# Kernel tuning notes

Hardware: AMD Instinct MI355X
Metric: run time of the kernel (lower is better)

The kernel has to match this reference:

```python
import jax, jax.numpy as jnp
import numpy as np

NUM_CLASSES = 80
LAMBDA_OBJ, LAMBDA_NOOBJ, LAMBDA_BBOX, LAMBDA_CLASS = 1.0, 0.5, 5.0, 1.0
IOU_POS = 0.5
ALPHA, GAMMA = 0.25, 2.0


def setup_inputs() -> dict:
    key = jax.random.key(0)
    ks = jax.random.split(key, 7)
    B, A, H, W, C, M = 8, 3, 80, 80, NUM_CLASSES, 100
    objectness = jax.random.uniform(ks[0], (B, A, H, W, 1), dtype=jnp.float32)
    xy = jax.random.uniform(ks[1], (B, A, H, W, 2), dtype=jnp.float32)
    wh = 0.05 + 0.25 * jax.random.uniform(ks[2], (B, A, H, W, 2), dtype=jnp.float32)
    boxes = jnp.concatenate([xy, wh], axis=-1)  # (cx,cy,w,h)
    class_scores = jax.random.normal(ks[3], (B, A, H, W, C), dtype=jnp.float32)
    txy = jax.random.uniform(ks[4], (B, M, 2), dtype=jnp.float32)
    twh = 0.05 + 0.25 * jax.random.uniform(ks[5], (B, M, 2), dtype=jnp.float32)
    target_boxes = jnp.concatenate([txy, twh], axis=-1)
    target_labels = jax.random.randint(ks[6], (B, M), 0, C)
    return {"objectness": objectness, "boxes": boxes, "class_scores": class_scores,
            "target_boxes": target_boxes, "target_labels": target_labels}


def _box_iou(b1, b2):
    # b1: [N,4], b2: [M,4] in (cx,cy,w,h) -> IoU [N,M]
    b1_lo = b1[:, :2] - b1[:, 2:] * 0.5
    b1_hi = b1[:, :2] + b1[:, 2:] * 0.5
    b2_lo = b2[:, :2] - b2[:, 2:] * 0.5
    b2_hi = b2[:, :2] + b2[:, 2:] * 0.5
    lo = jnp.maximum(b1_lo[:, None, :], b2_lo[None, :, :])
    hi = jnp.minimum(b1_hi[:, None, :], b2_hi[None, :, :])
    wh = jnp.clip(hi - lo, 0.0)
    inter = wh[..., 0] * wh[..., 1]
    a1 = b1[:, 2] * b1[:, 3]
    a2 = b2[:, 2] * b2[:, 3]
    union = a1[:, None] + a2[None, :] - inter
    return inter / (union + 1e-6)


def _giou(b1, b2):
    # elementwise pairs [N,4],[N,4] -> [N]
    b1_lo = b1[:, :2] - b1[:, 2:] * 0.5
    b1_hi = b1[:, :2] + b1[:, 2:] * 0.5
    b2_lo = b2[:, :2] - b2[:, 2:] * 0.5
    b2_hi = b2[:, :2] + b2[:, 2:] * 0.5
    wh = jnp.clip(jnp.minimum(b1_hi, b2_hi) - jnp.maximum(b1_lo, b2_lo), 0.0)
    inter = wh[:, 0] * wh[:, 1]
    union = b1[:, 2] * b1[:, 3] + b2[:, 2] * b2[:, 3] - inter
    iou = inter / (union + 1e-6)
    ewh = jnp.clip(jnp.maximum(b1_hi, b2_hi) - jnp.minimum(b1_lo, b2_lo), 0.0)
    enclose = ewh[:, 0] * ewh[:, 1]
    return iou - (enclose - union) / (enclose + 1e-6)


def _per_image(obj, boxes, cls, tb, tl):
    # obj:[N], boxes:[N,4], cls:[N,C], tb:[M,4], tl:[M]
    N = boxes.shape[0]
    iou = _box_iou(boxes, tb)                 # [N,M] -- dominant intermediate
    max_iou = jnp.max(iou, axis=1)
    idx = jnp.argmax(iou, axis=1)
    pos = max_iou >= IOU_POS
    posf = pos.astype(boxes.dtype)
    bbox_t = tb[idx] * posf[:, None]          # zeros for negatives
    class_t = jnp.where(pos, tl[idx], 0)
    # objectness BCE (torch BCELoss clamps log terms at -100), summed over anchors
    logp = jnp.maximum(jnp.log(obj), -100.0)
    log1mp = jnp.maximum(jnp.log1p(-obj), -100.0)
    bce_sum = -jnp.sum(posf * logp + (1.0 - posf) * log1mp)
    pos_cnt = jnp.sum(posf)
    # faithful to source: scalar BCE sum broadcast over masks then re-summed
    obj_term = bce_sum * (LAMBDA_OBJ * pos_cnt + LAMBDA_NOOBJ * (N - pos_cnt))
    # GIoU bbox loss over positive anchors
    giou = _giou(boxes, bbox_t)
    bbox_sum = jnp.sum((1.0 - giou) * posf)
    # focal loss (logits) vs one-hot, mean over positive subset [P,C]
    onehot = jax.nn.one_hot(class_t, NUM_CLASSES, dtype=cls.dtype)
    p = jax.nn.sigmoid(cls)
    ce = jnp.maximum(cls, 0.0) - cls * onehot + jnp.log1p(jnp.exp(-jnp.abs(cls)))
    p_t = p * onehot + (1.0 - p) * (1.0 - onehot)
    a_t = ALPHA * onehot + (1.0 - ALPHA) * (1.0 - onehot)
    fl = a_t * (1.0 - p_t) ** GAMMA * ce
    class_sum = jnp.sum(fl * posf[:, None]) / jnp.maximum(pos_cnt * NUM_CLASSES, 1.0)
    return obj_term, bbox_sum, class_sum, pos_cnt


def _forward(objectness, boxes, class_scores, target_boxes, target_labels):
    B = objectness.shape[0]
    obj_f = objectness.reshape(B, -1)
    box_f = boxes.reshape(B, -1, 4)
    cls_f = class_scores.reshape(B, -1, NUM_CLASSES)
    o, bb, cl, pc = jax.vmap(_per_image)(obj_f, box_f, cls_f, target_boxes, target_labels)
    num_pos = jnp.maximum(jnp.sum(pc), 1.0)
    obj_loss = jnp.sum(o) / B
    bbox_loss = LAMBDA_BBOX * jnp.sum(bb) / num_pos
    class_loss = LAMBDA_CLASS * jnp.sum(cl) / B
    return obj_loss + bbox_loss + class_loss


def reference(objectness, boxes, class_scores, target_boxes, target_labels):
    return _forward(objectness, boxes, class_scores, target_boxes, target_labels)
```

## Files before the change

kernel.cpp:

```cpp
#include <hip/hip_runtime.h>
#include <math.h>

#define NCLS    80
#define MTGT    100
#define NANCH   19200
#define BATCH   8
#define BLKA    64
#define NBLK    (NANCH / BLKA)
#define NWAVE   4
#define TSLICE  (MTGT / NWAVE)

__device__ __forceinline__ float fast_rcp(float x) { return __builtin_amdgcn_rcpf(x); }

__device__ __forceinline__ float focal_term(float x, bool is_t) {
    const float ax  = fabsf(x);
    const float q   = __expf(-ax);
    const float ce0 = fmaxf(x, 0.0f) + __logf(1.0f + q);
    const float r   = fast_rcp(1.0f + q);
    const float p   = (x >= 0.0f) ? r : q * r;
    const float pt  = is_t ? (1.0f - p) : p;
    const float ce  = is_t ? (ce0 - x) : ce0;
    const float at  = is_t ? 0.25f : 0.75f;
    return at * pt * pt * ce;
}

__global__ __launch_bounds__(256) void anchor_kernel(
    const float* __restrict__ obj, const float* __restrict__ boxes,
    const float* __restrict__ cls, const float* __restrict__ tb,
    const int* __restrict__ tl, float4* __restrict__ partials)
{
    __shared__ float4 t_box[MTGT];
    __shared__ float  t_area[MTGT];
    __shared__ int    t_lab[MTGT];
    __shared__ float  m_bi[NWAVE][BLKA];
    __shared__ float  m_bu[NWAVE][BLKA];
    __shared__ int    m_ix[NWAVE][BLKA];

    const int b    = blockIdx.y;
    const int tid  = threadIdx.x;
    const int wave = tid >> 6;
    const int lane = tid & 63;

    if (tid < MTGT) {
        const float4 t = ((const float4*)tb)[b * MTGT + tid];
        t_box[tid]  = make_float4(t.x - 0.5f * t.z, t.y - 0.5f * t.w,
                                  t.x + 0.5f * t.z, t.y + 0.5f * t.w);
        t_area[tid] = t.z * t.w;
        t_lab[tid]  = tl[b * MTGT + tid];
    }
    __syncthreads();

    const int a   = blockIdx.x * BLKA + lane;
    const int gid = b * NANCH + a;

    const float4 bx = ((const float4*)boxes)[gid];
    const float lox = bx.x - 0.5f * bx.z, loy = bx.y - 0.5f * bx.w;
    const float hix = bx.x + 0.5f * bx.z, hiy = bx.y + 0.5f * bx.w;
    const float a1  = bx.z * bx.w;
    const float aa  = a1 + 1e-6f;

    float bi = -1.0f, bu = 1.0f; int bidx = 0;
    const int m0 = wave * TSLICE;
    #pragma unroll
    for (int mm = 0; mm < TSLICE; ++mm) {
        const int m = m0 + mm;
        const float4 t = t_box[m];
        float iw = fmaxf(fminf(hix, t.z) - fmaxf(lox, t.x), 0.0f);
        float ih = fmaxf(fminf(hiy, t.w) - fmaxf(loy, t.y), 0.0f);
        float inter = iw * ih;
        float uni   = aa + t_area[m] - inter;
        if (inter * bu > bi * uni) { bi = inter; bu = uni; bidx = m; }
    }
    m_bi[wave][lane] = bi;
    m_bu[wave][lane] = bu;
    m_ix[wave][lane] = bidx;
    __syncthreads();

    if (wave != 0) return;

    float Bi = m_bi[0][lane], Bu = m_bu[0][lane]; int Bx = m_ix[0][lane];
    #pragma unroll
    for (int w = 1; w < NWAVE; ++w) {
        const float ci = m_bi[w][lane], cu = m_bu[w][lane];
        if (ci * Bu > Bi * cu) { Bi = ci; Bu = cu; Bx = m_ix[w][lane]; }
    }

    const bool  pos  = (Bi + Bi >= Bu);
    const float posf = pos ? 1.0f : 0.0f;

    const float o   = obj[gid];
    const float bce = -fmaxf(__logf(pos ? o : 1.0f - o), -100.0f);

    float bbox_l = 0.0f;
    float focal  = 0.0f;
    if (pos) {
        const float4 t   = t_box[Bx];
        const float uni  = a1 + t_area[Bx] - Bi;
        const float iou  = Bi * fast_rcp(Bu);
        const float ew   = fmaxf(fmaxf(hix, t.z) - fminf(lox, t.x), 0.0f);
        const float eh   = fmaxf(fmaxf(hiy, t.w) - fminf(loy, t.y), 0.0f);
        const float enc  = ew * eh;
        const float giou = iou - (enc - uni) * fast_rcp(enc + 1e-6f);
        bbox_l = 1.0f - giou;

        const int c = t_lab[Bx];
        const float4* row = (const float4*)(cls + (long)gid * NCLS);
        #pragma unroll
        for (int j4 = 0; j4 < NCLS / 4; ++j4) {
            const float4 v = row[j4];
            focal += focal_term(v.x, 4 * j4 + 0 == c);
            focal += focal_term(v.y, 4 * j4 + 1 == c);
            focal += focal_term(v.z, 4 * j4 + 2 == c);
            focal += focal_term(v.w, 4 * j4 + 3 == c);
        }
    }

    float v0 = bce, v1 = posf, v2 = bbox_l, v3 = focal;
    #pragma unroll
    for (int off = 32; off; off >>= 1) {
        v0 += __shfl_down(v0, off);
        v1 += __shfl_down(v1, off);
        v2 += __shfl_down(v2, off);
        v3 += __shfl_down(v3, off);
    }
    if (lane == 0)
        partials[b * NBLK + blockIdx.x] = make_float4(v0, v1, v2, v3);
}

__global__ __launch_bounds__(512) void finalize_kernel(
    const float4* __restrict__ partials, float* __restrict__ out)
{
    const int wave = threadIdx.x >> 6;
    const int lane = threadIdx.x & 63;

    float s0 = 0.f, s1 = 0.f, s2 = 0.f, s3 = 0.f;
    for (int blk = lane; blk < NBLK; blk += 64) {
        const float4 p = partials[wave * NBLK + blk];
        s0 += p.x; s1 += p.y; s2 += p.z; s3 += p.w;
    }
    #pragma unroll
    for (int off = 32; off; off >>= 1) {
        s0 += __shfl_down(s0, off);
        s1 += __shfl_down(s1, off);
        s2 += __shfl_down(s2, off);
        s3 += __shfl_down(s3, off);
    }
    __shared__ float img[BATCH][4];
    if (lane == 0) { img[wave][0] = s0; img[wave][1] = s1; img[wave][2] = s2; img[wave][3] = s3; }
    __syncthreads();
    if (threadIdx.x == 0) {
        float sum_pc = 0.f, obj_l = 0.f, bbox_s = 0.f, cls_l = 0.f;
        #pragma unroll
        for (int b = 0; b < BATCH; ++b) {
            const float bce = img[b][0];
            const float pc  = img[b][1];
            const float bb  = img[b][2];
            const float fo  = img[b][3];
            sum_pc += pc;
            obj_l  += bce * (1.0f * pc + 0.5f * ((float)NANCH - pc));
            bbox_s += bb;
            cls_l  += fo / fmaxf(pc * (float)NCLS, 1.0f);
        }
        const float num_pos = fmaxf(sum_pc, 1.0f);
        out[0] = obj_l / (float)BATCH + 5.0f * bbox_s / num_pos + cls_l / (float)BATCH;
    }
}

extern "C" void kernel_launch(void* const* d_in, const int* in_sizes, int n_in,
                              void* d_out, int out_size, void* d_ws, size_t ws_size,
                              hipStream_t stream) {
    const float* obj   = (const float*)d_in[0];
    const float* boxes = (const float*)d_in[1];
    const float* cls   = (const float*)d_in[2];
    const float* tb    = (const float*)d_in[3];
    const int*   tl    = (const int*)d_in[4];
    float* out = (float*)d_out;

    float4* partials = (float4*)d_ws;

    dim3 gridA(NBLK, BATCH);
    anchor_kernel<<<gridA, 256, 0, stream>>>(obj, boxes, cls, tb, tl, partials);
    finalize_kernel<<<1, 512, 0, stream>>>(partials, out);
}
```

Baseline: 115.1 us.

## Spread focal-loss class-row work across all four waves with coalesced loads

The focal class loss for positive anchors now runs on all 256 threads instead of only wave 0. Each thread handles a flat (anchor, float4-chunk) index, so the 64x80 class block is read with coalesced vector loads. Wave 0 still does the argmax merge, BCE and GIoU, and publishes per-anchor positive flags and labels through shared memory. This adds an extra barrier and a shared-memory reduction in exchange for better load coalescing and less serial per-thread work.

```diff
diff --git a/kernel.cpp b/kernel.cpp
--- a/kernel.cpp
+++ b/kernel.cpp
@@ -9,6 +9,7 @@
 #define NBLK    (NANCH / BLKA)
 #define NWAVE   4
 #define TSLICE  (MTGT / NWAVE)
+#define ROW4    (NCLS / 4)
 
 __device__ __forceinline__ float fast_rcp(float x) { return __builtin_amdgcn_rcpf(x); }
 
@@ -35,6 +36,10 @@
     __shared__ float  m_bi[NWAVE][BLKA];
     __shared__ float  m_bu[NWAVE][BLKA];
     __shared__ int    m_ix[NWAVE][BLKA];
+    __shared__ float  s_posf[BLKA];
+    __shared__ int    s_lab[BLKA];
+    __shared__ float  s_foc[NWAVE];
+    __shared__ float  s_bpb[3];
 
     const int b    = blockIdx.y;
     const int tid  = threadIdx.x;
@@ -50,8 +55,8 @@
     }
     __syncthreads();
 
-    const int a   = blockIdx.x * BLKA + lane;
-    const int gid = b * NANCH + a;
+    const int a0  = blockIdx.x * BLKA;
+    const int gid = b * NANCH + a0 + lane;
 
     const float4 bx = ((const float4*)boxes)[gid];
     const float lox = bx.x - 0.5f * bx.z, loy = bx.y - 0.5f * bx.w;
@@ -76,55 +81,74 @@
     m_ix[wave][lane] = bidx;
     __syncthreads();
 
-    if (wave != 0) return;
-
-    float Bi = m_bi[0][lane], Bu = m_bu[0][lane]; int Bx = m_ix[0][lane];
-    #pragma unroll
-    for (int w = 1; w < NWAVE; ++w) {
-        const float ci = m_bi[w][lane], cu = m_bu[w][lane];
-        if (ci * Bu > Bi * cu) { Bi = ci; Bu = cu; Bx = m_ix[w][lane]; }
-    }
-
-    const bool  pos  = (Bi + Bi >= Bu);
-    const float posf = pos ? 1.0f : 0.0f;
-
-    const float o   = obj[gid];
-    const float bce = -fmaxf(__logf(pos ? o : 1.0f - o), -100.0f);
-
-    float bbox_l = 0.0f;
-    float focal  = 0.0f;
-    if (pos) {
-        const float4 t   = t_box[Bx];
-        const float uni  = a1 + t_area[Bx] - Bi;
-        const float iou  = Bi * fast_rcp(Bu);
-        const float ew   = fmaxf(fmaxf(hix, t.z) - fminf(lox, t.x), 0.0f);
-        const float eh   = fmaxf(fmaxf(hiy, t.w) - fminf(loy, t.y), 0.0f);
-        const float enc  = ew * eh;
-        const float giou = iou - (enc - uni) * fast_rcp(enc + 1e-6f);
-        bbox_l = 1.0f - giou;
-
-        const int c = t_lab[Bx];
-        const float4* row = (const float4*)(cls + (long)gid * NCLS);
+    if (wave == 0) {
+        float Bi = m_bi[0][lane], Bu = m_bu[0][lane]; int Bx = m_ix[0][lane];
         #pragma unroll
-        for (int j4 = 0; j4 < NCLS / 4; ++j4) {
-            const float4 v = row[j4];
-            focal += focal_term(v.x, 4 * j4 + 0 == c);
-            focal += focal_term(v.y, 4 * j4 + 1 == c);
-            focal += focal_term(v.z, 4 * j4 + 2 == c);
-            focal += focal_term(v.w, 4 * j4 + 3 == c);
-        }
-    }
-
-    float v0 = bce, v1 = posf, v2 = bbox_l, v3 = focal;
-    #pragma unroll
-    for (int off = 32; off; off >>= 1) {
-        v0 += __shfl_down(v0, off);
-        v1 += __shfl_down(v1, off);
-        v2 += __shfl_down(v2, off);
-        v3 += __shfl_down(v3, off);
-    }
-    if (lane == 0)
-        partials[b * NBLK + blockIdx.x] = make_float4(v0, v1, v2, v3);
+        for (int w = 1; w < NWAVE; ++w) {
+            const float ci = m_bi[w][lane], cu = m_bu[w][lane];
+            if (ci * Bu > Bi * cu) { Bi = ci; Bu = cu; Bx = m_ix[w][lane]; }
+        }
+
+        const bool  pos  = (Bi + Bi >= Bu);
+        const float posf = pos ? 1.0f : 0.0f;
+        s_posf[lane] = posf;
+        s_lab[lane]  = t_lab[Bx];
+
+        const float o   = obj[gid];
+        const float bce = -fmaxf(__logf(pos ? o : 1.0f - o), -100.0f);
+
+        float bbox_l = 0.0f;
+        if (pos) {
+            const float4 t   = t_box[Bx];
+            const float uni  = a1 + t_area[Bx] - Bi;
+            const float iou  = Bi * fast_rcp(Bu);
+            const float ew   = fmaxf(fmaxf(hix, t.z) - fminf(lox, t.x), 0.0f);
+            const float eh   = fmaxf(fmaxf(hiy, t.w) - fminf(loy, t.y), 0.0f);
+            const float enc  = ew * eh;
+            const float giou = iou - (enc - uni) * fast_rcp(enc + 1e-6f);
+            bbox_l = 1.0f - giou;
+        }
+
+        float v0 = bce, v1 = posf, v2 = bbox_l;
+        #pragma unroll
+        for (int off = 32; off; off >>= 1) {
+            v0 += __shfl_down(v0, off);
+            v1 += __shfl_down(v1, off);
+            v2 += __shfl_down(v2, off);
+        }
+        if (lane == 0) { s_bpb[0] = v0; s_bpb[1] = v1; s_bpb[2] = v2; }
+    }
+    __syncthreads();
+
+    float focal = 0.0f;
+    #pragma unroll
+    for (int k = 0; k < 5; ++k) {
+        const int flat = k * 256 + tid;
+        const int a    = flat / ROW4;
+        const int j4   = flat - a * ROW4;
+        const float pf = s_posf[a];
+        if (pf != 0.0f) {
+            const int c = s_lab[a];
+            const float4 v = *(const float4*)(cls +
+                ((long)(b * NANCH + a0 + a)) * NCLS + j4 * 4);
+            float f = focal_term(v.x, 4 * j4 + 0 == c)
+                    + focal_term(v.y, 4 * j4 + 1 == c)
+                    + focal_term(v.z, 4 * j4 + 2 == c)
+                    + focal_term(v.w, 4 * j4 + 3 == c);
+            focal += f;
+        }
+    }
+    #pragma unroll
+    for (int off = 32; off; off >>= 1)
+        focal += __shfl_down(focal, off);
+    if (lane == 0) s_foc[wave] = focal;
+    __syncthreads();
+
+    if (tid == 0) {
+        const float fsum = s_foc[0] + s_foc[1] + s_foc[2] + s_foc[3];
+        partials[b * NBLK + blockIdx.x] =
+            make_float4(s_bpb[0], s_bpb[1], s_bpb[2], fsum);
+    }
 }
 
 __global__ __launch_bounds__(512) void finalize_kernel(
```

After: 109.5 us. 4.9% less time.
